# Optimization experiments

Measured on AMD Instinct MI355X. Metric: run time of the kernel, lower is better.

The kernel has to match this reference:

```python
import jax, jax.numpy as jnp
import numpy as np

B, C, K, D_SUB = 32768, 32, 256, 16
D_IN, D_OUT = C * D_SUB, 512


def setup_inputs() -> dict:
    key = jax.random.key(0)
    k1, k2, k3 = jax.random.split(key, 3)
    inputs = jax.random.normal(k1, (B, C, D_SUB), dtype=jnp.float32)
    centroids = jax.random.normal(k2, (C, K, D_SUB), dtype=jnp.float32)
    W = jax.random.normal(k3, (D_IN, D_OUT), dtype=jnp.float32) * (1.0 / np.sqrt(D_IN))
    return {"inputs": inputs, "centroids": centroids, "W": W}


def reference(inputs, centroids, W):
    # dot-metric response: (B, C, K). Equivalent to
    # torch.matmul(inputs.transpose(0,1), centroids.transpose(1,2)).transpose(0,1)
    response = jnp.einsum('bcd,ckd->bck', inputs, centroids)
    neg_mse = jnp.max(response, axis=-1)            # (B, C)
    codes = jnp.argmax(response, axis=-1)           # (B, C) int
    # codebook gather: outputs[b,c] = centroids[c, codes[b,c]]
    outputs = centroids[jnp.arange(C), codes]       # (B, C, D_SUB)
    # tie_in_n_out straight-through: value equals `outputs` in forward
    product = outputs.reshape(-1, C * D_SUB) @ W    # (B, D_OUT); fc has no bias
    return product, -neg_mse, codes
```

## Files before the change

### kernel.cpp

```cpp
#include <hip/hip_runtime.h>


#define NB 32768
#define NC 32
#define NK 256
#define NDS 16
#define NDIN 512
#define NDOUT 512
#define CERT 0.002f

typedef __attribute__((ext_vector_type(8))) short s8v;
typedef __attribute__((ext_vector_type(4))) float f4v;
typedef __attribute__((ext_vector_type(4))) unsigned int u4v;

__device__ __forceinline__ unsigned short f2bf(float f) {
  unsigned int u = __float_as_uint(f);
  u += 0x7fffu + ((u >> 16) & 1u);
  return (unsigned short)(u >> 16);
}
__device__ __forceinline__ float bf2f(unsigned short h) {
  return __uint_as_float(((unsigned int)h) << 16);
}

#define CVTPK(d, lo, hi) \
  asm("v_cvt_pk_bf16_f32 %0, %1, %2" : "=v"(d) : "v"(lo), "v"(hi))

__device__ __forceinline__ void gload16(const void* g, void* l) {
  __builtin_amdgcn_global_load_lds(
      (const __attribute__((address_space(1))) void*)g,
      (__attribute__((address_space(3))) void*)l, 16, 0, 0);
}

__device__ __forceinline__ float dot16(const float* x, const float* cj) {
  float4 a0 = *(const float4*)(x + 0),  a1 = *(const float4*)(x + 4);
  float4 a2 = *(const float4*)(x + 8),  a3 = *(const float4*)(x + 12);
  float4 c0 = *(const float4*)(cj + 0), c1 = *(const float4*)(cj + 4);
  float4 c2 = *(const float4*)(cj + 8), c3 = *(const float4*)(cj + 12);
  float s = a0.x * c0.x;
  s = fmaf(a0.y, c0.y, s); s = fmaf(a0.z, c0.z, s); s = fmaf(a0.w, c0.w, s);
  s = fmaf(a1.x, c1.x, s); s = fmaf(a1.y, c1.y, s); s = fmaf(a1.z, c1.z, s); s = fmaf(a1.w, c1.w, s);
  s = fmaf(a2.x, c2.x, s); s = fmaf(a2.y, c2.y, s); s = fmaf(a2.z, c2.z, s); s = fmaf(a2.w, c2.w, s);
  s = fmaf(a3.x, c3.x, s); s = fmaf(a3.y, c3.y, s); s = fmaf(a3.z, c3.z, s); s = fmaf(a3.w, c3.w, s);
  return s;
}

__global__ __launch_bounds__(256) void k_prep(const float* __restrict__ W,
                                              const float* __restrict__ cents,
                                              unsigned short* __restrict__ Wt,
                                              unsigned short* __restrict__ centsH,
                                              unsigned short* __restrict__ centsP4) {
  const int t = threadIdx.x;
  const int bid = blockIdx.x;
  if (bid < 256) {
    __shared__ float tile[32][33];
    const int k0 = (bid >> 4) << 5;
    const int n0 = (bid & 15) << 5;
    const int tx = t & 31, ty = t >> 5;
#pragma unroll
    for (int i = 0; i < 4; ++i) {
      int r = ty + i * 8;
      tile[r][tx] = W[(size_t)(k0 + r) * NDOUT + n0 + tx];
    }
    __syncthreads();
#pragma unroll
    for (int i = 0; i < 4; ++i) {
      int r = ty + i * 8;
      Wt[(size_t)(n0 + r) * NDIN + k0 + tx] = f2bf(tile[tx][r]);
    }
  } else {
    const int c = bid - 256;
    const int k = t;
    const float* src = cents + ((size_t)c * NK + k) * NDS;
    unsigned short hi[16], lo[16];
#pragma unroll
    for (int j = 0; j < 4; ++j) {
      float4 v = *(const float4*)(src + j * 4);
      unsigned short h0 = f2bf(v.x), h1 = f2bf(v.y), h2 = f2bf(v.z), h3 = f2bf(v.w);
      hi[j * 4 + 0] = h0; hi[j * 4 + 1] = h1; hi[j * 4 + 2] = h2; hi[j * 4 + 3] = h3;
      lo[j * 4 + 0] = f2bf(v.x - bf2f(h0));
      lo[j * 4 + 1] = f2bf(v.y - bf2f(h1));
      lo[j * 4 + 2] = f2bf(v.z - bf2f(h2));
      lo[j * 4 + 3] = f2bf(v.w - bf2f(h3));
    }
    unsigned short* hf = centsH + ((size_t)c * NK + k) * NDS;
#pragma unroll
    for (int j = 0; j < 4; ++j)
      *(ushort4*)(hf + j * 4) = make_ushort4(hi[j * 4], hi[j * 4 + 1], hi[j * 4 + 2], hi[j * 4 + 3]);
    unsigned short* pb = centsP4 + (size_t)c * 8192 + k * 8;
    *(ushort4*)(pb + 0 * 2048 + 0) = make_ushort4(hi[0], hi[1], hi[2], hi[3]);
    *(ushort4*)(pb + 0 * 2048 + 4) = make_ushort4(hi[4], hi[5], hi[6], hi[7]);
    *(ushort4*)(pb + 1 * 2048 + 0) = make_ushort4(hi[8], hi[9], hi[10], hi[11]);
    *(ushort4*)(pb + 1 * 2048 + 4) = make_ushort4(hi[12], hi[13], hi[14], hi[15]);
    *(ushort4*)(pb + 2 * 2048 + 0) = make_ushort4(lo[0], lo[1], lo[2], lo[3]);
    *(ushort4*)(pb + 2 * 2048 + 4) = make_ushort4(lo[4], lo[5], lo[6], lo[7]);
    *(ushort4*)(pb + 3 * 2048 + 0) = make_ushort4(lo[8], lo[9], lo[10], lo[11]);
    *(ushort4*)(pb + 3 * 2048 + 4) = make_ushort4(lo[12], lo[13], lo[14], lo[15]);
  }
}

__device__ __forceinline__ void split8(float4 u0, float4 u1, s8v& bh, s8v& bl) {
  unsigned int ph0, ph1, ph2, ph3;
  CVTPK(ph0, u0.x, u0.y); CVTPK(ph1, u0.z, u0.w);
  CVTPK(ph2, u1.x, u1.y); CVTPK(ph3, u1.z, u1.w);
  bh = __builtin_bit_cast(s8v, (u4v){ph0, ph1, ph2, ph3});
  float ra = u0.x - __uint_as_float(ph0 << 16);
  float rb = u0.y - __uint_as_float(ph0 & 0xFFFF0000u);
  float rc = u0.z - __uint_as_float(ph1 << 16);
  float rd = u0.w - __uint_as_float(ph1 & 0xFFFF0000u);
  float re = u1.x - __uint_as_float(ph2 << 16);
  float rf = u1.y - __uint_as_float(ph2 & 0xFFFF0000u);
  float rg = u1.z - __uint_as_float(ph3 << 16);
  float rh = u1.w - __uint_as_float(ph3 & 0xFFFF0000u);
  unsigned int pl0, pl1, pl2, pl3;
  CVTPK(pl0, ra, rb); CVTPK(pl1, rc, rd);
  CVTPK(pl2, re, rf); CVTPK(pl3, rg, rh);
  bl = __builtin_bit_cast(s8v, (u4v){pl0, pl1, pl2, pl3});
}

#define TRACK2(v0, v1, kc0, best, sec, bk)                     \
  {                                                            \
    float vm_ = fmaxf(v0, v1);                                 \
    float md_ = __builtin_amdgcn_fmed3f(best, v0, v1);         \
    sec = fmaxf(sec, md_);                                     \
    int km_ = (v1 > v0) ? (kc0 + 1) : (kc0);                   \
    bool gt_ = vm_ > best;                                     \
    bk = gt_ ? km_ : bk;                                       \
    best = fmaxf(best, vm_);                                   \
  }

__global__ __launch_bounds__(256, 4) void k_score(const float* __restrict__ inputs,
                                                  const unsigned short* __restrict__ centsP4,
                                                  const float* __restrict__ cents,
                                                  float* __restrict__ T_neg,
                                                  int* __restrict__ T_code) {
  const int t = threadIdx.x;
  const int l = t & 63;
  const int w = t >> 6;
  const int c = blockIdx.y;
  const int b0 = blockIdx.x * 128 + w * 32;
  const int g = l >> 4;
  const int col = l & 15;
  const int dh = (g & 1) * 8;
  const int g4 = g * 4;

  const float* r0 = inputs + ((size_t)(b0 + col) * NC + c) * NDS + dh;
  const float* r1 = inputs + ((size_t)(b0 + 16 + col) * NC + c) * NDS + dh;
  float4 u0 = *(const float4*)(r0), u1 = *(const float4*)(r0 + 4);
  float4 v0 = *(const float4*)(r1), v1 = *(const float4*)(r1 + 4);

  const unsigned short* abase = centsP4 + (size_t)c * 8192 + g * 2048 + col * 8;
  s8v areg[16];
#pragma unroll
  for (int kt = 0; kt < 16; ++kt)
    areg[kt] = *(const s8v*)(abase + kt * 128);

  s8v p1f0, p2f0, p1f1, p2f1;
  {
    s8v bh0, bl0, bh1, bl1;
    split8(u0, u1, bh0, bl0);
    split8(v0, v1, bh1, bl1);
    const bool hiLane = (l < 32);
    p1f0 = hiLane ? bh0 : bl0;
    p2f0 = hiLane ? bl0 : bh0;
    p1f1 = hiLane ? bh1 : bl1;
    p2f1 = hiLane ? bl1 : bh1;
  }

  float best0 = -3.0e38f, sec0 = -3.0e38f;
  float best1 = -3.0e38f, sec1 = -3.0e38f;
  int bk0 = 0, bk1 = 0;
  const f4v zz = {0.0f, 0.0f, 0.0f, 0.0f};

  __builtin_amdgcn_s_setprio(1);
#pragma unroll
  for (int kt = 0; kt < 16; ++kt) {
    s8v a = areg[kt];
    f4v acc0 = __builtin_amdgcn_mfma_f32_16x16x32_bf16(a, p1f0, zz, 0, 0, 0);
    acc0 = __builtin_amdgcn_mfma_f32_16x16x32_bf16(a, p2f0, acc0, 0, 0, 0);
    f4v acc1 = __builtin_amdgcn_mfma_f32_16x16x32_bf16(a, p1f1, zz, 0, 0, 0);
    acc1 = __builtin_amdgcn_mfma_f32_16x16x32_bf16(a, p2f1, acc1, 0, 0, 0);
    const int kc = kt * 16;
    TRACK2(acc0[0], acc0[1], kc + 0, best0, sec0, bk0)
    TRACK2(acc0[2], acc0[3], kc + 2, best0, sec0, bk0)
    TRACK2(acc1[0], acc1[1], kc + 0, best1, sec1, bk1)
    TRACK2(acc1[2], acc1[3], kc + 2, best1, sec1, bk1)
  }
  __builtin_amdgcn_s_setprio(0);

  bk0 += g4;
  bk1 += g4;

#pragma unroll
  for (int off = 16; off <= 32; off <<= 1) {
    float vb = __shfl_xor(best0, off);
    float sb = __shfl_xor(sec0, off);
    int kb = __shfl_xor(bk0, off);
    float mn = fminf(best0, vb);
    sec0 = fmaxf(fmaxf(sec0, sb), mn);
    bool take = (vb > best0) || (vb == best0 && kb < bk0);
    bk0 = take ? kb : bk0;
    best0 = fmaxf(best0, vb);

    vb = __shfl_xor(best1, off);
    sb = __shfl_xor(sec1, off);
    kb = __shfl_xor(bk1, off);
    mn = fminf(best1, vb);
    sec1 = fmaxf(fmaxf(sec1, sb), mn);
    take = (vb > best1) || (vb == best1 && kb < bk1);
    bk1 = take ? kb : bk1;
    best1 = fmaxf(best1, vb);
  }

  const int sub = (l >> 4) & 1;
  float best = sub ? best1 : best0;
  float sec = sub ? sec1 : sec0;
  int bk = sub ? bk1 : bk0;
  const bool owner = (l < 32);
  const bool flagged = owner && (best - sec <= CERT);

  if (owner && !flagged) {
    const int b = b0 + l;
    const float* xr = inputs + ((size_t)b * NC + c) * NDS;
    const float* cr = cents + ((size_t)c * NK + bk) * NDS;
    size_t o = (size_t)c * NB + b;
    T_neg[o] = dot16(xr, cr);
    T_code[o] = bk;
  }

  unsigned long long mask = __ballot(flagged);
  while (mask) {
    const int p = __builtin_ctzll(mask);
    mask &= mask - 1;
    const int b = b0 + p;
    const float* xr = inputs + ((size_t)b * NC + c) * NDS;
    const float* cr = cents + ((size_t)c * NK + l * 4) * NDS;
    float rb = -3.0e38f;
    int rk = 0;
#pragma unroll
    for (int q = 0; q < 4; ++q) {
      float d = dot16(xr, cr + q * NDS);
      if (d > rb) { rb = d; rk = l * 4 + q; }
    }
#pragma unroll
    for (int off = 1; off <= 32; off <<= 1) {
      float vb = __shfl_xor(rb, off);
      int kb = __shfl_xor(rk, off);
      bool take = (vb > rb) || (vb == rb && kb < rk);
      rb = take ? vb : rb;
      rk = take ? kb : rk;
    }
    if (l == 0) {
      size_t o = (size_t)c * NB + b;
      T_neg[o] = rb;
      T_code[o] = rk;
    }
  }
}

__global__ __launch_bounds__(256) void k_finish(const float* __restrict__ T_neg,
                                                const int* __restrict__ T_code,
                                                float* __restrict__ negout,
                                                float* __restrict__ codefout) {
  __shared__ float sneg[64][33];
  __shared__ int scode[64][33];
  const int t = threadIdx.x;
  const int b0 = blockIdx.x * 64;

#pragma unroll
  for (int it = 0; it < 8; ++it) {
    int lin = it * 256 + t;
    int c = lin >> 6, bi = lin & 63;
    sneg[bi][c] = T_neg[(size_t)c * NB + b0 + bi];
    scode[bi][c] = T_code[(size_t)c * NB + b0 + bi];
  }
  __syncthreads();

#pragma unroll
  for (int it = 0; it < 8; ++it) {
    int lin = it * 256 + t;
    int bi = lin >> 5, c = lin & 31;
    size_t o = (size_t)(b0 + bi) * NC + c;
    negout[o] = -sneg[bi][c];
    codefout[o] = (float)scode[bi][c];
  }
}

__global__ __launch_bounds__(256) void k_gemm(const unsigned short* __restrict__ centsB,
                                              const int* __restrict__ T_code,
                                              const unsigned short* __restrict__ Wt,
                                              float* __restrict__ out) {
  __shared__ __align__(16) unsigned short As[128 * 64];
  __shared__ __align__(16) unsigned short Bs[128 * 64];
  __shared__ int lcode[128 * 33];

  const int t = threadIdx.x;
  const int l = t & 63;
  const int w = t >> 6;
  const int wm = w >> 1, wn = w & 1;
  const int m0 = blockIdx.x * 128;
  const int n0 = blockIdx.y * 128;

  {
    const int cc = t >> 3;
    const int ch = t & 7;
#pragma unroll
    for (int i = 0; i < 4; ++i) {
      int row0 = ch * 16 + i * 4;
      int4 v = *(const int4*)(T_code + (size_t)cc * NB + m0 + row0);
      lcode[(row0 + 0) * 33 + cc] = v.x;
      lcode[(row0 + 1) * 33 + cc] = v.y;
      lcode[(row0 + 2) * 33 + cc] = v.z;
      lcode[(row0 + 3) * 33 + cc] = v.w;
    }
  }

  f4v acc[4][4] = {};
  const int s = t & 7;
  const int rq = t >> 3;

  for (int kt = 0; kt < 8; ++kt) {
    __syncthreads();
    const int c0 = kt * 4;
#pragma unroll
    for (int i = 0; i < 4; ++i) {
      int lr = i * 32 + rq;
      int srcslot = s ^ (lr & 7);
      int cl = srcslot >> 1, half = srcslot & 1;
      int code = lcode[lr * 33 + c0 + cl];
      const unsigned short* gsrc =
          centsB + ((size_t)((c0 + cl) * NK + code) * NDS + half * 8);
      gload16(gsrc, (char*)As + i * 4096 + (w << 10));
    }
#pragma unroll
    for (int i = 0; i < 4; ++i) {
      int lr = i * 32 + rq;
      int k16 = s ^ (lr & 7);
      const unsigned short* gsrc = Wt + (size_t)(n0 + lr) * NDIN + kt * 64 + k16 * 8;
      gload16(gsrc, (char*)Bs + i * 4096 + (w << 10));
    }
    __syncthreads();

    s8v af[4][2], bfr[4][2];
#pragma unroll
    for (int mf = 0; mf < 4; ++mf)
#pragma unroll
      for (int ks = 0; ks < 2; ++ks) {
        int row = wm * 64 + mf * 16 + (l & 15);
        int slot = ks * 4 + (l >> 4);
        af[mf][ks] = *(const s8v*)((const char*)As + row * 128 + ((slot ^ (row & 7)) << 4));
      }
#pragma unroll
    for (int nf = 0; nf < 4; ++nf)
#pragma unroll
      for (int ks = 0; ks < 2; ++ks) {
        int row = wn * 64 + nf * 16 + (l & 15);
        int slot = ks * 4 + (l >> 4);
        bfr[nf][ks] = *(const s8v*)((const char*)Bs + row * 128 + ((slot ^ (row & 7)) << 4));
      }
#pragma unroll
    for (int ks = 0; ks < 2; ++ks)
#pragma unroll
      for (int mf = 0; mf < 4; ++mf)
#pragma unroll
        for (int nf = 0; nf < 4; ++nf)
          acc[mf][nf] = __builtin_amdgcn_mfma_f32_16x16x32_bf16(
              af[mf][ks], bfr[nf][ks], acc[mf][nf], 0, 0, 0);
  }

#pragma unroll
  for (int mf = 0; mf < 4; ++mf)
#pragma unroll
    for (int nf = 0; nf < 4; ++nf)
#pragma unroll
      for (int r = 0; r < 4; ++r) {
        int row = m0 + wm * 64 + mf * 16 + (l >> 4) * 4 + r;
        int col = n0 + wn * 64 + nf * 16 + (l & 15);
        out[(size_t)row * NDOUT + col] = acc[mf][nf][r];
      }
}

extern "C" void kernel_launch(void* const* d_in, const int* in_sizes, int n_in,
                              void* d_out, int out_size, void* d_ws, size_t ws_size,
                              hipStream_t stream) {
  const float* inputs = (const float*)d_in[0];
  const float* cents  = (const float*)d_in[1];
  const float* W      = (const float*)d_in[2];

  float* out = (float*)d_out;
  float* negout   = out + (size_t)NB * NDOUT;
  float* codefout = negout + (size_t)NB * NC;

  unsigned short* Wt      = (unsigned short*)d_ws;
  unsigned short* centsH  = (unsigned short*)((char*)d_ws + 512 * 1024);
  unsigned short* centsP4 = (unsigned short*)((char*)d_ws + (1 << 20));
  float* T_neg            = (float*)((char*)d_ws + 2 * (1 << 20));
  int* T_code             = (int*)((char*)d_ws + 6 * (1 << 20));

  k_prep<<<288, 256, 0, stream>>>(W, cents, Wt, centsH, centsP4);
  k_score<<<dim3(NB / 128, NC), 256, 0, stream>>>(inputs, centsP4, cents, T_neg, T_code);
  k_finish<<<NB / 64, 256, 0, stream>>>(T_neg, T_code, negout, codefout);
  k_gemm<<<dim3(NB / 128, NDOUT / 128), 256, 0, stream>>>(centsH, T_code, Wt, out);
}
```

Baseline: 102.5 us.

## Process 64 rows per wave in k_score, reusing centroid fragments across four row tiles

Each wave in the scoring kernel now handles 64 batch rows instead of 32. Every loaded centroid fragment feeds four independent MFMA chains, and the grid is halved to match. Only 8 centroid fragments stay in registers at once, and the second half is loaded while the first half is being computed. The goal is more reuse of centroid loads and more independent MFMA work to hide latency, at the cost of extra registers for four sets of inputs and trackers, which may reduce occupancy. All 64 lanes now own a row in the epilogue.

```diff
diff --git a/kernel.cpp b/kernel.cpp
--- a/kernel.cpp
+++ b/kernel.cpp
@@ -128,6 +128,29 @@
     best = fmaxf(best, vm_);                                   \
   }
 
+#define CHAIN_STEP(a, p1, p2, kc, best, sec, bk)                             \
+  {                                                                          \
+    f4v acc_ = __builtin_amdgcn_mfma_f32_16x16x32_bf16(a, p1, zz, 0, 0, 0);  \
+    acc_ = __builtin_amdgcn_mfma_f32_16x16x32_bf16(a, p2, acc_, 0, 0, 0);    \
+    TRACK2(acc_[0], acc_[1], kc + 0, best, sec, bk)                          \
+    TRACK2(acc_[2], acc_[3], kc + 2, best, sec, bk)                          \
+  }
+
+#define BFLY(best, sec, bk)                                    \
+  {                                                            \
+    _Pragma("unroll")                                          \
+    for (int off = 16; off <= 32; off <<= 1) {                 \
+      float vb = __shfl_xor(best, off);                        \
+      float sb = __shfl_xor(sec, off);                         \
+      int kb = __shfl_xor(bk, off);                            \
+      float mn = fminf(best, vb);                              \
+      sec = fmaxf(fmaxf(sec, sb), mn);                         \
+      bool take = (vb > best) || (vb == best && kb < bk);      \
+      bk = take ? kb : bk;                                     \
+      best = fmaxf(best, vb);                                  \
+    }                                                          \
+  }
+
 __global__ __launch_bounds__(256, 4) void k_score(const float* __restrict__ inputs,
                                                   const unsigned short* __restrict__ centsP4,
                                                   const float* __restrict__ cents,
@@ -137,7 +160,7 @@
   const int l = t & 63;
   const int w = t >> 6;
   const int c = blockIdx.y;
-  const int b0 = blockIdx.x * 128 + w * 32;
+  const int b0 = blockIdx.x * 256 + w * 64;
   const int g = l >> 4;
   const int col = l & 15;
   const int dh = (g & 1) * 8;
@@ -145,80 +168,71 @@
 
   const float* r0 = inputs + ((size_t)(b0 + col) * NC + c) * NDS + dh;
   const float* r1 = inputs + ((size_t)(b0 + 16 + col) * NC + c) * NDS + dh;
-  float4 u0 = *(const float4*)(r0), u1 = *(const float4*)(r0 + 4);
-  float4 v0 = *(const float4*)(r1), v1 = *(const float4*)(r1 + 4);
+  const float* r2 = inputs + ((size_t)(b0 + 32 + col) * NC + c) * NDS + dh;
+  const float* r3 = inputs + ((size_t)(b0 + 48 + col) * NC + c) * NDS + dh;
+  float4 uA0 = *(const float4*)(r0), uA1 = *(const float4*)(r0 + 4);
+  float4 uB0 = *(const float4*)(r1), uB1 = *(const float4*)(r1 + 4);
+  float4 uC0 = *(const float4*)(r2), uC1 = *(const float4*)(r2 + 4);
+  float4 uD0 = *(const float4*)(r3), uD1 = *(const float4*)(r3 + 4);
 
   const unsigned short* abase = centsP4 + (size_t)c * 8192 + g * 2048 + col * 8;
-  s8v areg[16];
-#pragma unroll
-  for (int kt = 0; kt < 16; ++kt)
+  s8v areg[8];
+#pragma unroll
+  for (int kt = 0; kt < 8; ++kt)
     areg[kt] = *(const s8v*)(abase + kt * 128);
 
-  s8v p1f0, p2f0, p1f1, p2f1;
+  s8v p1A, p2A, p1B, p2B, p1C, p2C, p1D, p2D;
   {
-    s8v bh0, bl0, bh1, bl1;
-    split8(u0, u1, bh0, bl0);
-    split8(v0, v1, bh1, bl1);
+    s8v bh, bl;
     const bool hiLane = (l < 32);
-    p1f0 = hiLane ? bh0 : bl0;
-    p2f0 = hiLane ? bl0 : bh0;
-    p1f1 = hiLane ? bh1 : bl1;
-    p2f1 = hiLane ? bl1 : bh1;
-  }
-
-  float best0 = -3.0e38f, sec0 = -3.0e38f;
-  float best1 = -3.0e38f, sec1 = -3.0e38f;
-  int bk0 = 0, bk1 = 0;
+    split8(uA0, uA1, bh, bl); p1A = hiLane ? bh : bl; p2A = hiLane ? bl : bh;
+    split8(uB0, uB1, bh, bl); p1B = hiLane ? bh : bl; p2B = hiLane ? bl : bh;
+    split8(uC0, uC1, bh, bl); p1C = hiLane ? bh : bl; p2C = hiLane ? bl : bh;
+    split8(uD0, uD1, bh, bl); p1D = hiLane ? bh : bl; p2D = hiLane ? bl : bh;
+  }
+
+  float bestA = -3.0e38f, secA = -3.0e38f;
+  float bestB = -3.0e38f, secB = -3.0e38f;
+  float bestC = -3.0e38f, secC = -3.0e38f;
+  float bestD = -3.0e38f, secD = -3.0e38f;
+  int bkA = 0, bkB = 0, bkC = 0, bkD = 0;
   const f4v zz = {0.0f, 0.0f, 0.0f, 0.0f};
 
   __builtin_amdgcn_s_setprio(1);
 #pragma unroll
-  for (int kt = 0; kt < 16; ++kt) {
+  for (int kt = 0; kt < 8; ++kt) {
     s8v a = areg[kt];
-    f4v acc0 = __builtin_amdgcn_mfma_f32_16x16x32_bf16(a, p1f0, zz, 0, 0, 0);
-    acc0 = __builtin_amdgcn_mfma_f32_16x16x32_bf16(a, p2f0, acc0, 0, 0, 0);
-    f4v acc1 = __builtin_amdgcn_mfma_f32_16x16x32_bf16(a, p1f1, zz, 0, 0, 0);
-    acc1 = __builtin_amdgcn_mfma_f32_16x16x32_bf16(a, p2f1, acc1, 0, 0, 0);
+    areg[kt] = *(const s8v*)(abase + (kt + 8) * 128);
     const int kc = kt * 16;
-    TRACK2(acc0[0], acc0[1], kc + 0, best0, sec0, bk0)
-    TRACK2(acc0[2], acc0[3], kc + 2, best0, sec0, bk0)
-    TRACK2(acc1[0], acc1[1], kc + 0, best1, sec1, bk1)
-    TRACK2(acc1[2], acc1[3], kc + 2, best1, sec1, bk1)
+    CHAIN_STEP(a, p1A, p2A, kc, bestA, secA, bkA)
+    CHAIN_STEP(a, p1B, p2B, kc, bestB, secB, bkB)
+    CHAIN_STEP(a, p1C, p2C, kc, bestC, secC, bkC)
+    CHAIN_STEP(a, p1D, p2D, kc, bestD, secD, bkD)
+  }
+#pragma unroll
+  for (int kt = 8; kt < 16; ++kt) {
+    s8v a = areg[kt - 8];
+    const int kc = kt * 16;
+    CHAIN_STEP(a, p1A, p2A, kc, bestA, secA, bkA)
+    CHAIN_STEP(a, p1B, p2B, kc, bestB, secB, bkB)
+    CHAIN_STEP(a, p1C, p2C, kc, bestC, secC, bkC)
+    CHAIN_STEP(a, p1D, p2D, kc, bestD, secD, bkD)
   }
   __builtin_amdgcn_s_setprio(0);
 
-  bk0 += g4;
-  bk1 += g4;
-
-#pragma unroll
-  for (int off = 16; off <= 32; off <<= 1) {
-    float vb = __shfl_xor(best0, off);
-    float sb = __shfl_xor(sec0, off);
-    int kb = __shfl_xor(bk0, off);
-    float mn = fminf(best0, vb);
-    sec0 = fmaxf(fmaxf(sec0, sb), mn);
-    bool take = (vb > best0) || (vb == best0 && kb < bk0);
-    bk0 = take ? kb : bk0;
-    best0 = fmaxf(best0, vb);
-
-    vb = __shfl_xor(best1, off);
-    sb = __shfl_xor(sec1, off);
-    kb = __shfl_xor(bk1, off);
-    mn = fminf(best1, vb);
-    sec1 = fmaxf(fmaxf(sec1, sb), mn);
-    take = (vb > best1) || (vb == best1 && kb < bk1);
-    bk1 = take ? kb : bk1;
-    best1 = fmaxf(best1, vb);
-  }
-
-  const int sub = (l >> 4) & 1;
-  float best = sub ? best1 : best0;
-  float sec = sub ? sec1 : sec0;
-  int bk = sub ? bk1 : bk0;
-  const bool owner = (l < 32);
-  const bool flagged = owner && (best - sec <= CERT);
-
-  if (owner && !flagged) {
+  bkA += g4; bkB += g4; bkC += g4; bkD += g4;
+
+  BFLY(bestA, secA, bkA)
+  BFLY(bestB, secB, bkB)
+  BFLY(bestC, secC, bkC)
+  BFLY(bestD, secD, bkD)
+
+  float best = (g == 0) ? bestA : (g == 1) ? bestB : (g == 2) ? bestC : bestD;
+  float sec  = (g == 0) ? secA  : (g == 1) ? secB  : (g == 2) ? secC  : secD;
+  int bk     = (g == 0) ? bkA   : (g == 1) ? bkB   : (g == 2) ? bkC   : bkD;
+  const bool flagged = (best - sec <= CERT);
+
+  if (!flagged) {
     const int b = b0 + l;
     const float* xr = inputs + ((size_t)b * NC + c) * NDS;
     const float* cr = cents + ((size_t)c * NK + bk) * NDS;
@@ -397,7 +411,7 @@
   int* T_code             = (int*)((char*)d_ws + 6 * (1 << 20));
 
   k_prep<<<288, 256, 0, stream>>>(W, cents, Wt, centsH, centsP4);
-  k_score<<<dim3(NB / 128, NC), 256, 0, stream>>>(inputs, centsP4, cents, T_neg, T_code);
+  k_score<<<dim3(NB / 256, NC), 256, 0, stream>>>(inputs, centsP4, cents, T_neg, T_code);
   k_finish<<<NB / 64, 256, 0, stream>>>(T_neg, T_code, negout, codefout);
   k_gemm<<<dim3(NB / 128, NDOUT / 128), 256, 0, stream>>>(centsH, T_code, Wt, out);
 }
```

Measured after the change: 100.1 us. 1.02x faster.
